# Kernel optimization log

Measured on AMD Instinct MI355X. Metric: run time of the kernel, lower is better.

Reference implementation:

```python
import jax, jax.numpy as jnp
import numpy as np

B, S, D, F_DIM, E, TOP_K = 4, 2048, 1024, 1024, 8, 2


def setup_inputs() -> dict:
    key = jax.random.key(0)
    ks = jax.random.split(key, 6)
    return {
        "x": jax.random.normal(ks[0], (B, S, D), jnp.float32),
        "router_w": jax.random.normal(ks[1], (E, D), jnp.float32) * 0.02,
        "router_b": jax.random.normal(ks[2], (E,), jnp.float32) * 0.02,
        "expert_w": jax.random.normal(ks[3], (E, F_DIM, D), jnp.float32) * 0.02,
        "expert_b": jax.random.normal(ks[4], (E, F_DIM), jnp.float32) * 0.02,
        "expert_pref": jax.random.normal(ks[5], (E, D), jnp.float32),
        "top_k": TOP_K,
    }


def reference(x, router_w, router_b, expert_w, expert_b, expert_pref, top_k):
    num_experts = expert_w.shape[0]
    # Router: softmax over experts, then top-k with renormalization
    logits = jnp.einsum("bsd,ed->bse", x, router_w) + router_b
    routing_weights = jax.nn.softmax(logits, axis=-1)            # [B,S,E]
    top_w, top_idx = jax.lax.top_k(routing_weights, top_k)       # [B,S,K]
    top_w = top_w / jnp.sum(top_w, axis=-1, keepdims=True)
    # Dense per-expert combine weight: sum of renormalized top-k weights routed to each expert
    onehot = jax.nn.one_hot(top_idx, num_experts, dtype=x.dtype)  # [B,S,K,E]
    comb = jnp.einsum("bske,bsk->bse", onehot, top_w)             # [B,S,E]
    # Per-expert linear for every token, weighted combine (dense grouped-GEMM form)
    expert_out = jnp.einsum("bsd,efd->bsef", x, expert_w) + expert_b  # [B,S,E,F]
    final_output = jnp.einsum("bsef,bse->bsf", expert_out, comb)      # [B,S,F]
    # Expert utilization: fraction of tokens whose top-k contains expert i
    mask = jnp.sum(onehot, axis=2) > 0                            # [B,S,E]
    expert_utilization = jnp.mean(mask.astype(x.dtype), axis=(0, 1))
    # Load balance loss: MSE of mean routing weight vs ideal uniform usage
    usage = jnp.mean(routing_weights, axis=(0, 1))
    load_balance_loss = jnp.mean((usage - 1.0 / num_experts) ** 2)
    # Diversity: mean pairwise L2 distance over concatenated expert params (fixed small E)
    flat = jnp.concatenate(
        [expert_w.reshape(num_experts, -1), expert_b, expert_pref], axis=1
    )  # [E, P]
    dists = [jnp.linalg.norm(flat[i] - flat[j])
             for i in range(num_experts) for j in range(i + 1, num_experts)]
    diversity_score = jnp.mean(jnp.stack(dists))
    return final_output, routing_weights, expert_utilization, load_balance_loss, diversity_score
```

## Files before the change

kernel.cpp:

```cpp
#include <hip/hip_runtime.h>
#include <stdint.h>

typedef unsigned short u16;
typedef __attribute__((ext_vector_type(4))) float f32x4;
typedef __attribute__((ext_vector_type(8))) short bf16x8;

#define NTOK 8192
#define DDIM 1024
#define FDIM 1024
#define NEXP 8
#define PCAP 8192
#define RBLK 512

__device__ __align__(256) u16 g_xb[NTOK * DDIM];
__device__ __align__(256) u16 g_wbf[NEXP * FDIM * DDIM];
__device__ __align__(256) float g_buf0[NTOK * FDIM];
__device__ __align__(256) float g_buf1[NTOK * FDIM];
__device__ __align__(256) int g_ptok[NEXP * PCAP];
__device__ __align__(256) float g_pw[NEXP * PCAP];
__device__ __align__(256) unsigned g_e01[NTOK];
__device__ __align__(256) float g_w0[NTOK];
__device__ __align__(256) float g_w1[NTOK];
__device__ __align__(256) float g_usage_part[RBLK * NEXP];
__device__ __align__(256) float g_gram_part[512 * 36];
__device__ int g_cnt[16];

__device__ __forceinline__ u16 f2bf(float f) {
  unsigned u = __builtin_bit_cast(unsigned, f);
  unsigned r = u + 0x7fffu + ((u >> 16) & 1u);
  return (u16)(r >> 16);
}

__device__ __forceinline__ void gload_lds16(const void* g, void* l) {
  __builtin_amdgcn_global_load_lds(
      (const __attribute__((address_space(1))) void*)g,
      (__attribute__((address_space(3))) void*)l, 16, 0, 0);
}

__global__ __launch_bounds__(256) void k_pre(const float* __restrict__ x,
                                             const float* __restrict__ rwg,
                                             const float* __restrict__ rb,
                                             const float* __restrict__ ew,
                                             const float* __restrict__ ebias,
                                             const float* __restrict__ epref,
                                             float* __restrict__ rwout) {
  const int tid = threadIdx.x;
  if (blockIdx.x >= RBLK) {
    const int bid = blockIdx.x - RBLK;
    const int P0 = FDIM * DDIM;
    const int PT = P0 + FDIM + DDIM;
    float g[36];
#pragma unroll
    for (int i = 0; i < 36; ++i) g[i] = 0.f;
    for (int k = bid * 256 + tid; k < PT; k += RBLK * 256) {
      float v[8];
      if (k < P0) {
#pragma unroll
        for (int e = 0; e < 8; ++e) v[e] = ew[(size_t)e * P0 + k];
#pragma unroll
        for (int e = 0; e < 8; ++e) g_wbf[(size_t)e * P0 + k] = f2bf(v[e]);
      } else if (k < P0 + FDIM) {
        int kk = k - P0;
#pragma unroll
        for (int e = 0; e < 8; ++e) v[e] = ebias[e * FDIM + kk];
      } else {
        int kk = k - P0 - FDIM;
#pragma unroll
        for (int e = 0; e < 8; ++e) v[e] = epref[e * DDIM + kk];
      }
      int idx = 0;
#pragma unroll
      for (int i = 0; i < 8; ++i)
#pragma unroll
        for (int j = i; j < 8; ++j) {
          g[idx] += v[i] * v[j];
          ++idx;
        }
    }
#pragma unroll
    for (int i = 0; i < 36; ++i) {
      float a = g[i];
#pragma unroll
      for (int s = 32; s; s >>= 1) a += __shfl_xor(a, s);
      g[i] = a;
    }
    __shared__ float gs[4][36];
    const int w = tid >> 6, lane = tid & 63;
    if (lane == 0) {
#pragma unroll
      for (int i = 0; i < 36; ++i) gs[w][i] = g[i];
    }
    __syncthreads();
    if (tid < 36)
      g_gram_part[bid * 36 + tid] = gs[0][tid] + gs[1][tid] + gs[2][tid] +
                                    gs[3][tid];
    return;
  }
  __shared__ __align__(16) float rw_lds[NEXP * DDIM];
  __shared__ float us[NEXP];
  const int w = tid >> 6, lane = tid & 63;
  {
    const float4* src = (const float4*)rwg;
    float4* dst = (float4*)rw_lds;
#pragma unroll
    for (int i = 0; i < 8; ++i) dst[tid + 256 * i] = src[tid + 256 * i];
  }
  if (tid < NEXP) us[tid] = 0.f;
  __syncthreads();

  float rbl[NEXP];
#pragma unroll
  for (int e = 0; e < NEXP; ++e) rbl[e] = rb[e];
  float uw[NEXP];
#pragma unroll
  for (int e = 0; e < NEXP; ++e) uw[e] = 0.f;

  for (int it = 0; it < 4; ++it) {
    const int t = blockIdx.x * 16 + w * 4 + it;
    const float4* xv = (const float4*)(x + (size_t)t * DDIM);
    float4 xv4[4];
#pragma unroll
    for (int j = 0; j < 4; ++j) xv4[j] = xv[lane + 64 * j];
    ushort4* xo = (ushort4*)(g_xb + (size_t)t * DDIM);
#pragma unroll
    for (int j = 0; j < 4; ++j) {
      float4 v = xv4[j];
      ushort4 o;
      o.x = f2bf(v.x); o.y = f2bf(v.y); o.z = f2bf(v.z); o.w = f2bf(v.w);
      xo[lane + 64 * j] = o;
    }
    float lg[NEXP];
#pragma unroll
    for (int e = 0; e < NEXP; ++e) {
      float a = 0.f;
#pragma unroll
      for (int j = 0; j < 4; ++j) {
        float4 r = *(const float4*)&rw_lds[e * DDIM + (lane + 64 * j) * 4];
        float4 v = xv4[j];
        a += v.x * r.x + v.y * r.y + v.z * r.z + v.w * r.w;
      }
      lg[e] = a;
    }
#pragma unroll
    for (int e = 0; e < NEXP; ++e) {
      float a = lg[e];
#pragma unroll
      for (int s = 32; s; s >>= 1) a += __shfl_xor(a, s);
      lg[e] = a + rbl[e];
    }
    float mx = lg[0];
#pragma unroll
    for (int e = 1; e < NEXP; ++e) mx = fmaxf(mx, lg[e]);
    float p[NEXP];
    float sm = 0.f;
#pragma unroll
    for (int e = 0; e < NEXP; ++e) {
      p[e] = expf(lg[e] - mx);
      sm += p[e];
    }
    float inv = 1.f / sm;
#pragma unroll
    for (int e = 0; e < NEXP; ++e) {
      p[e] *= inv;
      uw[e] += p[e];
    }
    int e0 = 0;
    float b0 = p[0];
#pragma unroll
    for (int e = 1; e < NEXP; ++e)
      if (p[e] > b0) { b0 = p[e]; e0 = e; }
    int e1 = -1;
    float b1 = -1.f;
#pragma unroll
    for (int e = 0; e < NEXP; ++e)
      if (e != e0 && p[e] > b1) { b1 = p[e]; e1 = e; }
    if (lane == 0) {
      float4* rw4 = (float4*)(rwout + (size_t)t * NEXP);
      rw4[0] = make_float4(p[0], p[1], p[2], p[3]);
      rw4[1] = make_float4(p[4], p[5], p[6], p[7]);
      float rn = 1.f / (b0 + b1);
      g_e01[t] = (unsigned)e0 | ((unsigned)e1 << 8);
      g_w0[t] = b0 * rn;
      g_w1[t] = b1 * rn;
    }
  }
  if (lane == 0) {
#pragma unroll
    for (int e = 0; e < NEXP; ++e) atomicAdd(&us[e], uw[e]);
  }
  __syncthreads();
  if (tid < NEXP) g_usage_part[blockIdx.x * NEXP + tid] = us[tid];
}

__global__ __launch_bounds__(256) void k_lists(float* __restrict__ out_util,
                                               float* __restrict__ out_lbl,
                                               float* __restrict__ out_div) {
  const int tid = threadIdx.x;
  if (blockIdx.x == 8) {
    __shared__ int hist[8];
    __shared__ float su[8][33];
    __shared__ float sg[36][5];
    if (tid < 8) hist[tid] = 0;
    __syncthreads();
    for (int t = tid; t < NTOK; t += 256) {
      unsigned rec = g_e01[t];
      atomicAdd(&hist[rec & 255u], 1);
      atomicAdd(&hist[(rec >> 8) & 255u], 1);
    }
    {
      int e = tid & 7, part = tid >> 3;
      float s = 0.f;
      for (int i = part; i < RBLK; i += 32) s += g_usage_part[i * NEXP + e];
      su[e][part] = s;
      int gi = tid >> 2, gp = tid & 3;
      if (gi < 36) {
        float gsum = 0.f;
        for (int i = gp; i < 512; i += 4) gsum += g_gram_part[i * 36 + gi];
        sg[gi][gp] = gsum;
      }
    }
    __syncthreads();
    if (tid < 8) {
      float s2 = 0.f;
#pragma unroll
      for (int i = 0; i < 32; ++i) s2 += su[tid][i];
      su[tid][32] = s2;
      out_util[tid] = (float)hist[tid] * (1.f / 8192.f);
    }
    if (tid < 36) sg[tid][4] = sg[tid][0] + sg[tid][1] + sg[tid][2] + sg[tid][3];
    __syncthreads();
    if (tid == 0) {
      float dv = 0.f;
#pragma unroll
      for (int e = 0; e < 8; ++e) {
        float u = su[e][32] * (1.f / 8192.f) - 0.125f;
        dv += u * u;
      }
      out_lbl[0] = dv * 0.125f;
    }
    if (tid < 64) {
      float ds = 0.f;
      if (tid < 28) {
        int c = tid, i = 0;
        while (c >= 7 - i) { c -= 7 - i; ++i; }
        int j = i + 1 + c;
        auto tri = [](int a2, int b2) {
          return a2 * 8 - (a2 * (a2 - 1)) / 2 + (b2 - a2);
        };
        float d2 = sg[tri(i, i)][4] + sg[tri(j, j)][4] - 2.f * sg[tri(i, j)][4];
        ds = sqrtf(fmaxf(d2, 0.f));
      }
#pragma unroll
      for (int s = 16; s; s >>= 1) ds += __shfl_xor(ds, s);
      if (tid == 0) out_div[0] = ds * (1.f / 28.f);
    }
    return;
  }
  const int e = blockIdx.x;
  const int wv = tid >> 6, lane = tid & 63;
  __shared__ int wcnt[4];
  int base = 0;
  for (int c = 0; c < NTOK / 256; ++c) {
    const int t = c * 256 + tid;
    unsigned rec = g_e01[t];
    int m0 = (int)(rec & 255u) == e;
    int m1 = (int)((rec >> 8) & 255u) == e;
    unsigned long long bal = __ballot(m0 || m1);
    int rank = __popcll(bal & ((1ull << lane) - 1ull));
    if (lane == 0) wcnt[wv] = __popcll(bal);
    __syncthreads();
    int pre = base;
#pragma unroll
    for (int i = 0; i < 4; ++i)
      if (i < wv) pre += wcnt[i];
    int tot = wcnt[0] + wcnt[1] + wcnt[2] + wcnt[3];
    if (m0 || m1) {
      int idx = pre + rank;
      g_ptok[e * PCAP + idx] = (t << 1) | (m1 ? 1 : 0);
      g_pw[e * PCAP + idx] = m1 ? g_w1[t] : g_w0[t];
    }
    base += tot;
    __syncthreads();
  }
  if (tid == 0) g_cnt[e] = base;
}

__global__ __launch_bounds__(512) void k_gemm(const float* __restrict__ eb) {
  int s = blockIdx.x;
  int e = 0;
  for (; e < NEXP; ++e) {
    int nt = (g_cnt[e] + 127) >> 7;
    if (s < nt) break;
    s -= nt;
  }
  if (e == NEXP) return;
  const int count = g_cnt[e];
  const int m0 = s * 128;
  const int n0 = blockIdx.y * 128;

  __shared__ __align__(16) u16 As[2][128 * 64];
  __shared__ __align__(16) u16 Bs[2][128 * 64];

  const int tid = threadIdx.x;
  const int lane = tid & 63;
  const int w = tid >> 6;
  const int wm = w >> 2, wn = w & 3;
  const int col16 = lane & 15, rg = lane >> 4;

  const int* ptok = g_ptok + e * PCAP;

  const u16* srcA[2];
  const u16* srcB[2];
  unsigned soff[2];
#pragma unroll
  for (int c = 0; c < 2; ++c) {
    int o = c * 8192 + tid * 16;
    int row = o >> 7;
    int sl = (o >> 4) & 7;
    int r = m0 + row;
    if (r > count - 1) r = count - 1;
    int tk = (ptok[r] >> 1) & (NTOK - 1);
    srcA[c] = g_xb + (size_t)tk * DDIM + ((sl ^ (row & 7)) << 3);
    srcB[c] = g_wbf + (size_t)e * (FDIM * DDIM) + (size_t)(n0 + row) * DDIM +
              ((sl ^ (row & 7)) << 3);
    soff[c] = (unsigned)o;
  }

#define STAGE(buf, k0)                                                        \
  {                                                                           \
    _Pragma("unroll") for (int c = 0; c < 2; ++c)                             \
        gload_lds16((const char*)(srcA[c] + (k0)), (char*)As[buf] + soff[c]); \
    _Pragma("unroll") for (int c = 0; c < 2; ++c)                             \
        gload_lds16((const char*)(srcB[c] + (k0)), (char*)Bs[buf] + soff[c]); \
  }

  f32x4 acc[4][2];
  const f32x4 zz = {0.f, 0.f, 0.f, 0.f};
#pragma unroll
  for (int i = 0; i < 4; ++i)
#pragma unroll
    for (int j = 0; j < 2; ++j) acc[i][j] = zz;

  STAGE(0, 0);
  STAGE(1, 64);

  const int sxor = col16 & 7;
  for (int kk = 0; kk < 16; ++kk) {
    const int cur = kk & 1;
    if (kk < 15) {
      asm volatile("s_waitcnt vmcnt(4)" ::: "memory");
    } else {
      asm volatile("s_waitcnt vmcnt(0)" ::: "memory");
    }
    __builtin_amdgcn_s_barrier();
    __builtin_amdgcn_sched_barrier(0);

#pragma unroll
    for (int ki = 0; ki < 2; ++ki) {
      bf16x8 af[4], bg[2];
#pragma unroll
      for (int mi = 0; mi < 4; ++mi) {
        int row = wm * 64 + mi * 16 + col16;
        af[mi] = *(const bf16x8*)(As[cur] + row * 64 +
                                  (((ki * 4 + rg) ^ sxor) << 3));
      }
#pragma unroll
      for (int ni = 0; ni < 2; ++ni) {
        int row = wn * 32 + ni * 16 + col16;
        bg[ni] = *(const bf16x8*)(Bs[cur] + row * 64 +
                                  (((ki * 4 + rg) ^ sxor) << 3));
      }
      __builtin_amdgcn_s_setprio(1);
#pragma unroll
      for (int mi = 0; mi < 4; ++mi)
#pragma unroll
        for (int ni = 0; ni < 2; ++ni)
          acc[mi][ni] = __builtin_amdgcn_mfma_f32_16x16x32_bf16(
              af[mi], bg[ni], acc[mi][ni], 0, 0, 0);
      __builtin_amdgcn_s_setprio(0);
    }

    asm volatile("" ::: "memory");
    __builtin_amdgcn_s_barrier();
    asm volatile("" ::: "memory");
    if (kk + 2 < 16) STAGE(cur, (kk + 2) * 64);
  }
#undef STAGE

#pragma unroll
  for (int mi = 0; mi < 4; ++mi) {
#pragma unroll
    for (int j = 0; j < 4; ++j) {
      int r = m0 + wm * 64 + mi * 16 + rg * 4 + j;
      if (r < count) {
        int enc = ptok[r];
        int tk = (enc >> 1) & (NTOK - 1);
        float wgt = g_pw[e * PCAP + r];
        float* dst = (enc & 1 ? g_buf1 : g_buf0) + (size_t)tk * FDIM + n0 +
                     wn * 32 + col16;
        const float* bias = eb + e * FDIM + n0 + wn * 32 + col16;
#pragma unroll
        for (int ni = 0; ni < 2; ++ni)
          dst[ni * 16] = wgt * (acc[mi][ni][j] + bias[ni * 16]);
      }
    }
  }
}

__global__ __launch_bounds__(256) void k_combine(float4* __restrict__ o, int n) {
  const float4* a = (const float4*)g_buf0;
  const float4* b = (const float4*)g_buf1;
  int i = blockIdx.x * 256 + threadIdx.x;
  int stride = gridDim.x * 256;
  for (; i < n; i += stride) {
    float4 va = a[i], vb = b[i];
    o[i] = make_float4(va.x + vb.x, va.y + vb.y, va.z + vb.z, va.w + vb.w);
  }
}

extern "C" void kernel_launch(void* const* d_in, const int* in_sizes, int n_in,
                              void* d_out, int out_size, void* d_ws,
                              size_t ws_size, hipStream_t stream) {
  const float* x = (const float*)d_in[0];
  const float* rwg = (const float*)d_in[1];
  const float* rb = (const float*)d_in[2];
  const float* ew = (const float*)d_in[3];
  const float* eb = (const float*)d_in[4];
  const float* ep = (const float*)d_in[5];

  float* out = (float*)d_out;
  float* out_final = out;
  float* out_rw = out + (size_t)NTOK * FDIM;
  float* out_util = out_rw + (size_t)NTOK * NEXP;
  float* out_lbl = out_util + NEXP;
  float* out_div = out_lbl + 1;

  k_pre<<<1024, 256, 0, stream>>>(x, rwg, rb, ew, eb, ep, out_rw);
  k_lists<<<9, 256, 0, stream>>>(out_util, out_lbl, out_div);
  k_gemm<<<dim3(136, 8), 512, 0, stream>>>(eb);
  k_combine<<<2048, 256, 0, stream>>>((float4*)out_final, (NTOK * FDIM) / 4);
}
```

Baseline: 151.5 us.

## Store expert partial outputs in bf16 and interleave GEMM tiles across experts

The per-slot intermediate buffers written by the expert GEMM and read by the combine kernel change from fp32 to bf16, halving that scratch traffic. The combine kernel unpacks bf16 pairs and sums them into fp32 output. The tile-to-expert mapping is now precomputed in k_lists as a round-robin interleave across experts instead of a linear scan inside each GEMM block, which spreads experts across concurrently running blocks. The cost is extra rounding error in the final output from the bf16 intermediates.

```diff
diff --git a/kernel.cpp b/kernel.cpp
--- a/kernel.cpp
+++ b/kernel.cpp
@@ -14,8 +14,8 @@
 
 __device__ __align__(256) u16 g_xb[NTOK * DDIM];
 __device__ __align__(256) u16 g_wbf[NEXP * FDIM * DDIM];
-__device__ __align__(256) float g_buf0[NTOK * FDIM];
-__device__ __align__(256) float g_buf1[NTOK * FDIM];
+__device__ __align__(256) u16 g_buf0[NTOK * FDIM];
+__device__ __align__(256) u16 g_buf1[NTOK * FDIM];
 __device__ __align__(256) int g_ptok[NEXP * PCAP];
 __device__ __align__(256) float g_pw[NEXP * PCAP];
 __device__ __align__(256) unsigned g_e01[NTOK];
@@ -23,12 +23,17 @@
 __device__ __align__(256) float g_w1[NTOK];
 __device__ __align__(256) float g_usage_part[RBLK * NEXP];
 __device__ __align__(256) float g_gram_part[512 * 36];
+__device__ __align__(256) unsigned g_tile[160];
 __device__ int g_cnt[16];
 
 __device__ __forceinline__ u16 f2bf(float f) {
   unsigned u = __builtin_bit_cast(unsigned, f);
   unsigned r = u + 0x7fffu + ((u >> 16) & 1u);
   return (u16)(r >> 16);
+}
+
+__device__ __forceinline__ float b2f(unsigned h) {
+  return __builtin_bit_cast(float, h << 16);
 }
 
 __device__ __forceinline__ void gload_lds16(const void* g, void* l) {
@@ -237,6 +242,22 @@
         dv += u * u;
       }
       out_lbl[0] = dv * 0.125f;
+      int nt[8], placed[8];
+#pragma unroll
+      for (int e = 0; e < 8; ++e) {
+        nt[e] = (hist[e] + 127) >> 7;
+        placed[e] = 0;
+      }
+      for (int p = 0; p < 136; ++p) {
+        int e = p & 7;
+        if (placed[e] >= nt[e]) {
+          e = -1;
+          for (int f = 0; f < 8; ++f)
+            if (placed[f] < nt[f]) { e = f; break; }
+        }
+        g_tile[p] = (e < 0) ? 0xFFFFFFFFu
+                            : (((unsigned)e << 16) | (unsigned)placed[e]++);
+      }
     }
     if (tid < 64) {
       float ds = 0.f;
@@ -286,16 +307,12 @@
 }
 
 __global__ __launch_bounds__(512) void k_gemm(const float* __restrict__ eb) {
-  int s = blockIdx.x;
-  int e = 0;
-  for (; e < NEXP; ++e) {
-    int nt = (g_cnt[e] + 127) >> 7;
-    if (s < nt) break;
-    s -= nt;
-  }
-  if (e == NEXP) return;
+  const unsigned tl = g_tile[blockIdx.x];
+  if (tl == 0xFFFFFFFFu) return;
+  const int e = tl >> 16;
   const int count = g_cnt[e];
-  const int m0 = s * 128;
+  const int m0 = (tl & 0xffffu) * 128;
+  if (m0 >= count) return;
   const int n0 = blockIdx.y * 128;
 
   __shared__ __align__(16) u16 As[2][128 * 64];
@@ -396,25 +413,35 @@
         int enc = ptok[r];
         int tk = (enc >> 1) & (NTOK - 1);
         float wgt = g_pw[e * PCAP + r];
-        float* dst = (enc & 1 ? g_buf1 : g_buf0) + (size_t)tk * FDIM + n0 +
-                     wn * 32 + col16;
+        u16* dst = (enc & 1 ? g_buf1 : g_buf0) + (size_t)tk * FDIM + n0 +
+                   wn * 32 + col16;
         const float* bias = eb + e * FDIM + n0 + wn * 32 + col16;
 #pragma unroll
         for (int ni = 0; ni < 2; ++ni)
-          dst[ni * 16] = wgt * (acc[mi][ni][j] + bias[ni * 16]);
-      }
-    }
-  }
-}
-
-__global__ __launch_bounds__(256) void k_combine(float4* __restrict__ o, int n) {
-  const float4* a = (const float4*)g_buf0;
-  const float4* b = (const float4*)g_buf1;
+          dst[ni * 16] = f2bf(wgt * (acc[mi][ni][j] + bias[ni * 16]));
+      }
+    }
+  }
+}
+
+__global__ __launch_bounds__(256) void k_combine(float4* __restrict__ o, int n8) {
+  const uint4* a = (const uint4*)g_buf0;
+  const uint4* b = (const uint4*)g_buf1;
   int i = blockIdx.x * 256 + threadIdx.x;
   int stride = gridDim.x * 256;
-  for (; i < n; i += stride) {
-    float4 va = a[i], vb = b[i];
-    o[i] = make_float4(va.x + vb.x, va.y + vb.y, va.z + vb.z, va.w + vb.w);
+  for (; i < n8; i += stride) {
+    uint4 va = a[i], vb = b[i];
+    float4 lo, hi;
+    lo.x = b2f(va.x & 0xffffu) + b2f(vb.x & 0xffffu);
+    lo.y = b2f(va.x >> 16) + b2f(vb.x >> 16);
+    lo.z = b2f(va.y & 0xffffu) + b2f(vb.y & 0xffffu);
+    lo.w = b2f(va.y >> 16) + b2f(vb.y >> 16);
+    hi.x = b2f(va.z & 0xffffu) + b2f(vb.z & 0xffffu);
+    hi.y = b2f(va.z >> 16) + b2f(vb.z >> 16);
+    hi.z = b2f(va.w & 0xffffu) + b2f(vb.w & 0xffffu);
+    hi.w = b2f(va.w >> 16) + b2f(vb.w >> 16);
+    o[(size_t)i * 2] = lo;
+    o[(size_t)i * 2 + 1] = hi;
   }
 }
 
@@ -438,5 +465,5 @@
   k_pre<<<1024, 256, 0, stream>>>(x, rwg, rb, ew, eb, ep, out_rw);
   k_lists<<<9, 256, 0, stream>>>(out_util, out_lbl, out_div);
   k_gemm<<<dim3(136, 8), 512, 0, stream>>>(eb);
-  k_combine<<<2048, 256, 0, stream>>>((float4*)out_final, (NTOK * FDIM) / 4);
-}
+  k_combine<<<2048, 256, 0, stream>>>((float4*)out_final, (NTOK * FDIM) / 8);
+}
```

Measured after the change: 162.3 us. 7.1% more time.
